# Kernel optimization log

Measured on AMD Instinct MI355X. Metric: run time of the kernel, lower is better.

## Reference

```python
import jax, jax.numpy as jnp
import numpy as np

HID = 256


def _mlp(h, ws, bs):
    # 4-layer MLP: tanh x3, sigmoid output (matches nn.Sequential in torch code)
    h = jnp.tanh(h @ ws[0] + bs[0])
    h = jnp.tanh(h @ ws[1] + bs[1])
    h = jnp.tanh(h @ ws[2] + bs[2])
    return jax.nn.sigmoid(h @ ws[3] + bs[3])


def setup_inputs() -> dict:
    key = jax.random.key(0)
    N, K, DE = 100000, 32, 8
    IN1 = K * DE          # 256
    MID = 5
    IN2 = K * MID         # 160
    E = N * K
    ks = jax.random.split(key, 20)
    x = jax.random.normal(ks[0], (N, DE), dtype=jnp.float32)
    edge_index = jax.random.randint(ks[1], (2, E), 0, N, dtype=jnp.int64)
    edge_attr = jax.random.normal(ks[2], (E, DE), dtype=jnp.float32)

    def lin(k, fan_in, fan_out):
        kw, kb = jax.random.split(k)
        lim = 1.0 / np.sqrt(fan_in)
        w = jax.random.uniform(kw, (fan_in, fan_out), jnp.float32, -lim, lim)
        b = jax.random.uniform(kb, (fan_out,), jnp.float32, -lim, lim)
        return w, b

    dims1 = [(IN1, HID), (HID, HID), (HID, HID), (HID, MID)]
    dims2 = [(IN2, HID), (HID, HID), (HID, HID), (HID, 1)]
    inp = {"x": x, "edge_index": edge_index, "edge_attr": edge_attr}
    for i, (fi, fo) in enumerate(dims1):
        w, b = lin(ks[3 + i], fi, fo)
        inp[f"w1_{i}"], inp[f"b1_{i}"] = w, b
    for i, (fi, fo) in enumerate(dims2):
        w, b = lin(ks[10 + i], fi, fo)
        inp[f"w2_{i}"], inp[f"b2_{i}"] = w, b
    return inp


def reference(x, edge_index, edge_attr,
              w1_0, b1_0, w1_1, b1_1, w1_2, b1_2, w1_3, b1_3,
              w2_0, b2_0, w2_1, b2_1, w2_2, b2_2, w2_3, b2_3):
    K = 32
    IN1 = w1_0.shape[0]              # 256
    MID = w1_3.shape[1]              # 5
    # GNN1: message = edge_attr; aggregate reshapes to [N, IN1] then MLP -> [N, MID]
    out1 = _mlp(edge_attr.reshape(-1, IN1), (w1_0, w1_1, w1_2, w1_3), (b1_0, b1_1, b1_2, b1_3))
    # GNN2: message = x_j = out1[edge_index[1]] (flow='target_to_source')
    gathered = out1[edge_index[1]]                     # [E, MID] irregular gather
    out2 = _mlp(gathered.reshape(-1, K * MID), (w2_0, w2_1, w2_2, w2_3), (b2_0, b2_1, b2_2, b2_3))
    return out2[:, 0]                                  # squeeze dim 1 -> [N]
```

## Files before the change

### kernel.cpp

```cpp
#include <hip/hip_runtime.h>
#include <stdint.h>

typedef uint16_t u16;
typedef uint32_t u32;
typedef __attribute__((ext_vector_type(8)))  __bf16 bf16x8;
typedef __attribute__((ext_vector_type(16))) float  f32x16;

#define NROWS   100000
#define E_EDGES 3200000

#define HIDX(r, g) (((r) << 8) + ((((g) ^ ((r) & 31))) << 3))

#define MFMA(a, b, c) __builtin_amdgcn_mfma_f32_32x32x16_bf16((a), (b), (c), 0, 0, 0)

__device__ __forceinline__ u32 pk_bf16(float a, float b) {
    u32 ua = __builtin_bit_cast(u32, a), ub = __builtin_bit_cast(u32, b);
    ua = (ua + 0x7FFFu + ((ua >> 16) & 1u)) >> 16;
    ub = (ub + 0x7FFFu + ((ub >> 16) & 1u)) >> 16;
    return ua | (ub << 16);
}
__device__ __forceinline__ float fast_tanh(float x) {
    float e = __expf(2.0f * x);
    return 1.0f - __fdividef(2.0f, e + 1.0f);
}
__device__ __forceinline__ float fast_sigmoid(float x) {
    return __fdividef(1.0f, 1.0f + __expf(-x));
}

__device__ __forceinline__ void load_w16(bf16x8 (&W)[16], const u16* __restrict__ base,
                                         int stride) {
#pragma unroll
    for (int s = 0; s < 16; ++s) W[s] = *(const bf16x8*)(base + s * stride);
}

__device__ __forceinline__ void dense_layer(const u16* __restrict__ Hin, u16* __restrict__ Hout,
                                            bf16x8 (&W)[16], const u16* __restrict__ pfbase,
                                            int pfstride, const float* __restrict__ bias,
                                            int nt, int l31, int lh) {
    f32x16 acc0, acc1;
#pragma unroll
    for (int j = 0; j < 16; ++j) { acc0[j] = 0.0f; acc1[j] = 0.0f; }

#pragma unroll
    for (int s = 0; s < 16; ++s) {
        const int g = 2 * s + lh;
        bf16x8 h0 = *(const bf16x8*)(Hin + HIDX(l31, g));
        bf16x8 h1 = *(const bf16x8*)(Hin + HIDX(32 + l31, g));
        acc0 = MFMA(W[s], h0, acc0);
        acc1 = MFMA(W[s], h1, acc1);
        W[s] = *(const bf16x8*)(pfbase + s * pfstride);
    }
#pragma unroll
    for (int rg = 0; rg < 4; ++rg) {
        const float4 bv = *(const float4*)(bias + nt * 32 + rg * 8 + lh * 4);
#pragma unroll
        for (int b = 0; b < 2; ++b) {
            const f32x16& A = b ? acc1 : acc0;
            float x0 = fast_tanh(A[rg * 4 + 0] + bv.x);
            float x1 = fast_tanh(A[rg * 4 + 1] + bv.y);
            float x2 = fast_tanh(A[rg * 4 + 2] + bv.z);
            float x3 = fast_tanh(A[rg * 4 + 3] + bv.w);
            const int r = b * 32 + l31;
            const int g = nt * 4 + rg;
            uint2 v; v.x = pk_bf16(x0, x1); v.y = pk_bf16(x2, x3);
            *(uint2*)(Hout + (r << 8) + (((g) ^ (r & 31)) << 3) + lh * 4) = v;
        }
    }
}

__device__ __forceinline__ f32x16 final_dense(const u16* __restrict__ Hin, bf16x8 (&W)[16],
                                              int wave, int l31, int lh) {
    f32x16 acc;
#pragma unroll
    for (int j = 0; j < 16; ++j) acc[j] = 0.0f;
    if (wave < 2) {
#pragma unroll
        for (int s = 0; s < 16; ++s) {
            const int g = 2 * s + lh;
            bf16x8 h = *(const bf16x8*)(Hin + HIDX(wave * 32 + l31, g));
            acc = MFMA(W[s], h, acc);
        }
    }
    return acc;
}

__global__ __launch_bounds__(512, 4) void mlp1_kernel(
    const float* __restrict__ ea, const u16* __restrict__ WB1, const u16* __restrict__ WB13,
    const float* __restrict__ b0, const float* __restrict__ b1, const float* __restrict__ b2,
    const float* __restrict__ b3, u16* __restrict__ out1) {
    __shared__ u16 H0[64 * 256];
    __shared__ u16 H1[64 * 256];
    const int tid = threadIdx.x, wave = tid >> 6, lane = tid & 63, blk = blockIdx.x;
    const int l31 = lane & 31, lh = lane >> 5, nt = wave;
    const int woff = (nt * 32 + l31) * 16 + lh * 8;

    bf16x8 W[16];
    load_w16(W, WB1 + woff, 4096);

#pragma unroll
    for (int i = 0; i < 4; ++i) {
        const int r = i * 16 + (tid >> 5);
        const int g = tid & 31;
        const int rg_ = blk * 64 + r;
        uint4 v = {0u, 0u, 0u, 0u};
        if (rg_ < NROWS) {
            const float* p = ea + (size_t)rg_ * 256 + g * 8;
            float4 a0 = *(const float4*)p;
            float4 a1 = *(const float4*)(p + 4);
            v.x = pk_bf16(a0.x, a0.y); v.y = pk_bf16(a0.z, a0.w);
            v.z = pk_bf16(a1.x, a1.y); v.w = pk_bf16(a1.z, a1.w);
        }
        *(uint4*)(H0 + HIDX(r, g)) = v;
    }
    __syncthreads();
    dense_layer(H0, H1, W, WB1 + 65536  + woff, 4096, b0, nt, l31, lh);
    __syncthreads();
    dense_layer(H1, H0, W, WB1 + 131072 + woff, 4096, b1, nt, l31, lh);
    __syncthreads();
    dense_layer(H0, H1, W, WB13 + l31 * 16 + lh * 8, 512, b2, nt, l31, lh);
    __syncthreads();
    f32x16 acc = final_dense(H1, W, wave, l31, lh);

    if (wave < 2) {
        const int row_g = blk * 64 + wave * 32 + l31;
        if (row_g < NROWS) {
            if (lh == 0) {
                float s0 = fast_sigmoid(acc[0] + b3[0]);
                float s1 = fast_sigmoid(acc[1] + b3[1]);
                float s2 = fast_sigmoid(acc[2] + b3[2]);
                float s3 = fast_sigmoid(acc[3] + b3[3]);
                uint2 v; v.x = pk_bf16(s0, s1); v.y = pk_bf16(s2, s3);
                *(uint2*)(out1 + (size_t)row_g * 8) = v;
            } else {
                float s4 = fast_sigmoid(acc[0] + b3[4]);
                uint2 v; v.x = pk_bf16(s4, 0.0f); v.y = 0u;
                *(uint2*)(out1 + (size_t)row_g * 8 + 4) = v;
            }
        }
    }
}

__global__ __launch_bounds__(512, 4) void mlp2_kernel(
    const int* __restrict__ idx1, const u16* __restrict__ out1,
    const u16* __restrict__ WB2, const u16* __restrict__ WB23,
    const float* __restrict__ b0, const float* __restrict__ b1, const float* __restrict__ b2,
    const float* __restrict__ b3, float* __restrict__ out) {
    __shared__ u16 H0[64 * 256];
    __shared__ u16 H1[64 * 256];
    const int tid = threadIdx.x, wave = tid >> 6, lane = tid & 63, blk = blockIdx.x;
    const int l31 = lane & 31, lh = lane >> 5, nt = wave;
    const int woff = (nt * 32 + l31) * 16 + lh * 8;

    bf16x8 W[16];
    load_w16(W, WB2 + woff, 4096);

    int nodes[4];
#pragma unroll
    for (int i = 0; i < 4; ++i) {
        const long e = (long)blk * 2048 + i * 512 + tid;
        nodes[i] = (e < (long)E_EDGES) ? idx1[e] : -1;
    }
#pragma unroll
    for (int i = 0; i < 4; ++i) {
        const int li = i * 512 + tid;
        const int r = li >> 5, j = li & 31;
        uint4 v = {0u, 0u, 0u, 0u};
        if (nodes[i] >= 0) v = *(const uint4*)(out1 + (size_t)nodes[i] * 8);
        *(uint4*)(H0 + HIDX(r, j)) = v;
    }
    __syncthreads();
    dense_layer(H0, H1, W, WB2 + 65536  + woff, 4096, b0, nt, l31, lh);
    __syncthreads();
    dense_layer(H1, H0, W, WB2 + 131072 + woff, 4096, b1, nt, l31, lh);
    __syncthreads();
    dense_layer(H0, H1, W, WB23 + l31 * 16 + lh * 8, 512, b2, nt, l31, lh);
    __syncthreads();
    f32x16 acc = final_dense(H1, W, wave, l31, lh);

    if (wave < 2) {
        const int row_g = blk * 64 + wave * 32 + l31;
        if (row_g < NROWS && lh == 0)
            out[row_g] = fast_sigmoid(acc[0] + b3[0]);
    }
}

__global__ void transform_kernel(
    const float* __restrict__ w10, const float* __restrict__ w11, const float* __restrict__ w12,
    const float* __restrict__ w13, const float* __restrict__ w20, const float* __restrict__ w21,
    const float* __restrict__ w22, const float* __restrict__ w23, u16* __restrict__ ws) {
    const int id = blockIdx.x * 256 + threadIdx.x;
    float val;
    if (id < 196608) {
        int layer = id >> 16, rem = id & 65535;
        int c = rem >> 13, s = (rem >> 12) & 1, n = (rem >> 4) & 255, kl = rem & 15;
        int k = c * 32 + s * 16 + kl;
        const float* w = layer == 0 ? w10 : (layer == 1 ? w11 : w12);
        val = w[k * 256 + n];
    } else if (id < 204800) {
        int rem = id - 196608;
        int c = rem >> 10, s = (rem >> 9) & 1, n = (rem >> 4) & 31, kl = rem & 15;
        int k = c * 32 + s * 16 + kl;
        val = (n < 5) ? w13[k * 5 + n] : 0.0f;
    } else if (id < 401408) {
        int rem = id - 204800;
        int layer = rem >> 16; rem &= 65535;
        int c = rem >> 13, s = (rem >> 12) & 1, n = (rem >> 4) & 255, kl = rem & 15;
        int k = c * 32 + s * 16 + kl;
        if (layer == 0) {
            int j = k >> 3, v = k & 7;
            val = (v < 5) ? w20[(j * 5 + v) * 256 + n] : 0.0f;
        } else {
            val = (layer == 1 ? w21 : w22)[k * 256 + n];
        }
    } else {
        int rem = id - 401408;
        int c = rem >> 10, s = (rem >> 9) & 1, n = (rem >> 4) & 31, kl = rem & 15;
        int k = c * 32 + s * 16 + kl;
        val = (n == 0) ? w23[k] : 0.0f;
    }
    u32 u = __builtin_bit_cast(u32, val);
    u = (u + 0x7FFFu + ((u >> 16) & 1u)) >> 16;
    ws[id] = (u16)u;
}

extern "C" void kernel_launch(void* const* d_in, const int* in_sizes, int n_in,
                              void* d_out, int out_size, void* d_ws, size_t ws_size,
                              hipStream_t stream) {
    const int*   ei  = (const int*)d_in[1];
    const float* ea  = (const float*)d_in[2];
    const float* w10 = (const float*)d_in[3];  const float* b10 = (const float*)d_in[4];
    const float* w11 = (const float*)d_in[5];  const float* b11 = (const float*)d_in[6];
    const float* w12 = (const float*)d_in[7];  const float* b12 = (const float*)d_in[8];
    const float* w13 = (const float*)d_in[9];  const float* b13 = (const float*)d_in[10];
    const float* w20 = (const float*)d_in[11]; const float* b20 = (const float*)d_in[12];
    const float* w21 = (const float*)d_in[13]; const float* b21 = (const float*)d_in[14];
    const float* w22 = (const float*)d_in[15]; const float* b22 = (const float*)d_in[16];
    const float* w23 = (const float*)d_in[17]; const float* b23 = (const float*)d_in[18];

    u16* ws   = (u16*)d_ws;
    u16* WB1  = ws;
    u16* WB13 = ws + 196608;
    u16* WB2  = ws + 204800;
    u16* WB23 = ws + 401408;
    u16* out1 = ws + 409600;

    hipLaunchKernelGGL(transform_kernel, dim3(1600), dim3(256), 0, stream,
                       w10, w11, w12, w13, w20, w21, w22, w23, ws);
    hipLaunchKernelGGL(mlp1_kernel, dim3(1563), dim3(512), 0, stream,
                       ea, WB1, WB13, b10, b11, b12, b13, out1);
    hipLaunchKernelGGL(mlp2_kernel, dim3(1563), dim3(512), 0, stream,
                       ei + E_EDGES, out1, WB2, WB23, b20, b21, b22, b23, (float*)d_out);
}
```

Before: 364.2 us.

## Prefetch LDS activations, use hardware exp2/rcp, relax launch bounds

The dense layers now load the next K-step's activation fragments from LDS one iteration ahead of the MFMAs that consume them, so LDS latency overlaps matrix work. Tanh and sigmoid use the raw exp2 and reciprocal intrinsics in place of expf and fdividef. Launch bounds drop from 4 to 2 blocks per CU, which gives the compiler more registers but allows lower occupancy. The edge-attribute staging and the weight-transform index math are also rewritten; the transform simplification looks equivalent because c*32+s*16 equals the combined 4-bit s times 16.

```diff
diff --git a/kernel.cpp b/kernel.cpp
--- a/kernel.cpp
+++ b/kernel.cpp
@@ -13,18 +13,20 @@
 
 #define MFMA(a, b, c) __builtin_amdgcn_mfma_f32_32x32x16_bf16((a), (b), (c), 0, 0, 0)
 
-__device__ __forceinline__ u32 pk_bf16(float a, float b) {
+__device__ __forceinline__ u32 pk2(float a, float b) {
     u32 ua = __builtin_bit_cast(u32, a), ub = __builtin_bit_cast(u32, b);
     ua = (ua + 0x7FFFu + ((ua >> 16) & 1u)) >> 16;
     ub = (ub + 0x7FFFu + ((ub >> 16) & 1u)) >> 16;
     return ua | (ub << 16);
 }
 __device__ __forceinline__ float fast_tanh(float x) {
-    float e = __expf(2.0f * x);
-    return 1.0f - __fdividef(2.0f, e + 1.0f);
+    float e = __builtin_amdgcn_exp2f(x * 2.885390081777927f);
+    float r = __builtin_amdgcn_rcpf(e + 1.0f);
+    return __builtin_fmaf(-2.0f, r, 1.0f);
 }
 __device__ __forceinline__ float fast_sigmoid(float x) {
-    return __fdividef(1.0f, 1.0f + __expf(-x));
+    float e = __builtin_amdgcn_exp2f(x * -1.4426950408889634f);
+    return __builtin_amdgcn_rcpf(1.0f + e);
 }
 
 __device__ __forceinline__ void load_w16(bf16x8 (&W)[16], const u16* __restrict__ base,
@@ -41,14 +43,21 @@
 #pragma unroll
     for (int j = 0; j < 16; ++j) { acc0[j] = 0.0f; acc1[j] = 0.0f; }
 
+    bf16x8 h0 = *(const bf16x8*)(Hin + HIDX(l31, lh));
+    bf16x8 h1 = *(const bf16x8*)(Hin + HIDX(32 + l31, lh));
+
 #pragma unroll
     for (int s = 0; s < 16; ++s) {
-        const int g = 2 * s + lh;
-        bf16x8 h0 = *(const bf16x8*)(Hin + HIDX(l31, g));
-        bf16x8 h1 = *(const bf16x8*)(Hin + HIDX(32 + l31, g));
+        bf16x8 nh0 = h0, nh1 = h1;
+        if (s < 15) {
+            const int ng = 2 * (s + 1) + lh;
+            nh0 = *(const bf16x8*)(Hin + HIDX(l31, ng));
+            nh1 = *(const bf16x8*)(Hin + HIDX(32 + l31, ng));
+        }
         acc0 = MFMA(W[s], h0, acc0);
         acc1 = MFMA(W[s], h1, acc1);
         W[s] = *(const bf16x8*)(pfbase + s * pfstride);
+        h0 = nh0; h1 = nh1;
     }
 #pragma unroll
     for (int rg = 0; rg < 4; ++rg) {
@@ -62,7 +71,7 @@
             float x3 = fast_tanh(A[rg * 4 + 3] + bv.w);
             const int r = b * 32 + l31;
             const int g = nt * 4 + rg;
-            uint2 v; v.x = pk_bf16(x0, x1); v.y = pk_bf16(x2, x3);
+            uint2 v; v.x = pk2(x0, x1); v.y = pk2(x2, x3);
             *(uint2*)(Hout + (r << 8) + (((g) ^ (r & 31)) << 3) + lh * 4) = v;
         }
     }
@@ -74,17 +83,20 @@
 #pragma unroll
     for (int j = 0; j < 16; ++j) acc[j] = 0.0f;
     if (wave < 2) {
+        bf16x8 h = *(const bf16x8*)(Hin + HIDX(wave * 32 + l31, lh));
 #pragma unroll
         for (int s = 0; s < 16; ++s) {
-            const int g = 2 * s + lh;
-            bf16x8 h = *(const bf16x8*)(Hin + HIDX(wave * 32 + l31, g));
+            bf16x8 nh = h;
+            if (s < 15)
+                nh = *(const bf16x8*)(Hin + HIDX(wave * 32 + l31, 2 * (s + 1) + lh));
             acc = MFMA(W[s], h, acc);
+            h = nh;
         }
     }
     return acc;
 }
 
-__global__ __launch_bounds__(512, 4) void mlp1_kernel(
+__global__ __launch_bounds__(512, 2) void mlp1_kernel(
     const float* __restrict__ ea, const u16* __restrict__ WB1, const u16* __restrict__ WB13,
     const float* __restrict__ b0, const float* __restrict__ b1, const float* __restrict__ b2,
     const float* __restrict__ b3, u16* __restrict__ out1) {
@@ -99,16 +111,16 @@
 
 #pragma unroll
     for (int i = 0; i < 4; ++i) {
-        const int r = i * 16 + (tid >> 5);
-        const int g = tid & 31;
+        const int li = i * 512 + tid;
+        const int r = li >> 5, g = li & 31;
         const int rg_ = blk * 64 + r;
         uint4 v = {0u, 0u, 0u, 0u};
         if (rg_ < NROWS) {
             const float* p = ea + (size_t)rg_ * 256 + g * 8;
             float4 a0 = *(const float4*)p;
             float4 a1 = *(const float4*)(p + 4);
-            v.x = pk_bf16(a0.x, a0.y); v.y = pk_bf16(a0.z, a0.w);
-            v.z = pk_bf16(a1.x, a1.y); v.w = pk_bf16(a1.z, a1.w);
+            v.x = pk2(a0.x, a0.y); v.y = pk2(a0.z, a0.w);
+            v.z = pk2(a1.x, a1.y); v.w = pk2(a1.z, a1.w);
         }
         *(uint4*)(H0 + HIDX(r, g)) = v;
     }
@@ -129,18 +141,18 @@
                 float s1 = fast_sigmoid(acc[1] + b3[1]);
                 float s2 = fast_sigmoid(acc[2] + b3[2]);
                 float s3 = fast_sigmoid(acc[3] + b3[3]);
-                uint2 v; v.x = pk_bf16(s0, s1); v.y = pk_bf16(s2, s3);
+                uint2 v; v.x = pk2(s0, s1); v.y = pk2(s2, s3);
                 *(uint2*)(out1 + (size_t)row_g * 8) = v;
             } else {
                 float s4 = fast_sigmoid(acc[0] + b3[4]);
-                uint2 v; v.x = pk_bf16(s4, 0.0f); v.y = 0u;
+                uint2 v; v.x = pk2(s4, 0.0f); v.y = 0u;
                 *(uint2*)(out1 + (size_t)row_g * 8 + 4) = v;
             }
         }
     }
 }
 
-__global__ __launch_bounds__(512, 4) void mlp2_kernel(
+__global__ __launch_bounds__(512, 2) void mlp2_kernel(
     const int* __restrict__ idx1, const u16* __restrict__ out1,
     const u16* __restrict__ WB2, const u16* __restrict__ WB23,
     const float* __restrict__ b0, const float* __restrict__ b1, const float* __restrict__ b2,
@@ -192,20 +204,20 @@
     float val;
     if (id < 196608) {
         int layer = id >> 16, rem = id & 65535;
-        int c = rem >> 13, s = (rem >> 12) & 1, n = (rem >> 4) & 255, kl = rem & 15;
-        int k = c * 32 + s * 16 + kl;
+        int s = rem >> 12, n = (rem >> 4) & 255, kl = rem & 15;
+        int k = s * 16 + kl;
         const float* w = layer == 0 ? w10 : (layer == 1 ? w11 : w12);
         val = w[k * 256 + n];
     } else if (id < 204800) {
         int rem = id - 196608;
-        int c = rem >> 10, s = (rem >> 9) & 1, n = (rem >> 4) & 31, kl = rem & 15;
-        int k = c * 32 + s * 16 + kl;
+        int s = rem >> 9, n = (rem >> 4) & 31, kl = rem & 15;
+        int k = s * 16 + kl;
         val = (n < 5) ? w13[k * 5 + n] : 0.0f;
     } else if (id < 401408) {
         int rem = id - 204800;
         int layer = rem >> 16; rem &= 65535;
-        int c = rem >> 13, s = (rem >> 12) & 1, n = (rem >> 4) & 255, kl = rem & 15;
-        int k = c * 32 + s * 16 + kl;
+        int s = rem >> 12, n = (rem >> 4) & 255, kl = rem & 15;
+        int k = s * 16 + kl;
         if (layer == 0) {
             int j = k >> 3, v = k & 7;
             val = (v < 5) ? w20[(j * 5 + v) * 256 + n] : 0.0f;
@@ -214,8 +226,8 @@
         }
     } else {
         int rem = id - 401408;
-        int c = rem >> 10, s = (rem >> 9) & 1, n = (rem >> 4) & 31, kl = rem & 15;
-        int k = c * 32 + s * 16 + kl;
+        int s = rem >> 9, n = (rem >> 4) & 31, kl = rem & 15;
+        int k = s * 16 + kl;
         val = (n == 0) ? w23[k] : 0.0f;
     }
     u32 u = __builtin_bit_cast(u32, val);
```

After: 339.1 us. 6.9% less time.
